# Performance work log

Hardware: AMD Instinct MI355X
Metric: run time of the kernel (lower is better)

## Reference

```python
import jax, jax.numpy as jnp
import numpy as np

CD_WEIGHT = 100.0


def setup_inputs() -> dict:
    key = jax.random.key(0)
    k1, k2 = jax.random.split(key)
    array1 = jax.random.normal(k1, (4, 4096, 3), dtype=jnp.float32)
    array2 = jax.random.normal(k2, (4, 4096, 3), dtype=jnp.float32)
    return {"array1": array1, "array2": array2}


def _chamfer(a1, a2):
    # a1: [B, N, D], a2: [B, M, D]
    # squared pairwise distances d2[b, n, m] = ||a1[b,n] - a2[b,m]||^2
    # computed as ||a||^2 + ||b||^2 - 2 a.b to avoid materializing [B,N,M,D]
    sq1 = jnp.sum(a1 * a1, axis=-1)                      # [B, N]
    sq2 = jnp.sum(a2 * a2, axis=-1)                      # [B, M]
    cross = jnp.einsum("bnd,bmd->bnm", a1, a2)           # [B, N, M]
    d2 = sq1[:, :, None] + sq2[:, None, :] - 2.0 * cross  # [B, N, M]
    # av_dist1: for each array2 point, min over array1 points, then mean
    av_dist1 = jnp.mean(jnp.min(d2, axis=1), axis=-1)    # [B]
    # av_dist2: for each array1 point, min over array2 points, then mean
    av_dist2 = jnp.mean(jnp.min(d2, axis=2), axis=-1)    # [B]
    return CD_WEIGHT * jnp.mean(0.5 * (av_dist1 + av_dist2))


def reference(array1, array2):
    return _chamfer(array1, array2)
```

## Files before the change

kernel.cpp:

```cpp
#include <hip/hip_runtime.h>
#include <math.h>


#define NPTS     4096
#define NBATCH   4
#define RSPLIT   32
#define RCHUNK   (NPTS / RSPLIT)
#define QPB      256
#define QPT      8
#define QBLK     (QPB * QPT)
#define NQTOT    (2 * NBATCH * NPTS)
#define SCALE    (50.0f / (float)(NBATCH * NPTS))

__global__ __launch_bounds__(QPB) void chamfer_stage1(
    const float* __restrict__ a1, const float* __restrict__ a2,
    float* __restrict__ pm)
{
    __shared__ float4 refs[RCHUNK];

    const int b   = blockIdx.y;
    const int dir = blockIdx.z >> 5;
    const int c   = blockIdx.z & 31;
    const float* q = (dir == 0) ? a1 : a2;
    const float* r = (dir == 0) ? a2 : a1;
    q += (size_t)b * NPTS * 3;
    r += (size_t)b * NPTS * 3;

    if (threadIdx.x < RCHUNK) {
        const int g = c * RCHUNK + threadIdx.x;
        float rx = r[3 * g + 0];
        float ry = r[3 * g + 1];
        float rz = r[3 * g + 2];
        refs[threadIdx.x] = make_float4(rx, ry, rz, rx * rx + ry * ry + rz * rz);
    }

    const int q0 = blockIdx.x * QBLK + threadIdx.x;
    float qx2[QPT], qy2[QPT], qz2[QPT], q2[QPT];
    #pragma unroll
    for (int k = 0; k < QPT; ++k) {
        const int qi = q0 + k * QPB;
        float x = q[3 * qi + 0];
        float y = q[3 * qi + 1];
        float z = q[3 * qi + 2];
        q2[k]  = x * x + y * y + z * z;
        qx2[k] = -2.0f * x;
        qy2[k] = -2.0f * y;
        qz2[k] = -2.0f * z;
    }
    __syncthreads();

    float mins[QPT];
    #pragma unroll
    for (int k = 0; k < QPT; ++k) mins[k] = INFINITY;

    #pragma unroll 2
    for (int j = 0; j < RCHUNK; ++j) {
        float4 p = refs[j];
        #pragma unroll
        for (int k = 0; k < QPT; ++k) {
            float t = fmaf(qz2[k], p.z,
                      fmaf(qy2[k], p.y,
                      fmaf(qx2[k], p.x, p.w)));
            mins[k] = fminf(mins[k], t);
        }
    }

    const int qgbase = (dir * NBATCH + b) * NPTS + q0;
    #pragma unroll
    for (int k = 0; k < QPT; ++k) {
        pm[(size_t)c * NQTOT + qgbase + k * QPB] = mins[k] + q2[k];
    }
}

__global__ __launch_bounds__(256) void chamfer_stage2(
    const float* __restrict__ pm, float* __restrict__ psum)
{
    const int qg = blockIdx.x * 256 + threadIdx.x;
    float m = INFINITY;
    #pragma unroll
    for (int c = 0; c < RSPLIT; ++c)
        m = fminf(m, pm[(size_t)c * NQTOT + qg]);

    float s = m;
    for (int off = 32; off > 0; off >>= 1) s += __shfl_down(s, off);
    __shared__ float wsum[4];
    if ((threadIdx.x & 63) == 0) wsum[threadIdx.x >> 6] = s;
    __syncthreads();
    if (threadIdx.x == 0)
        psum[blockIdx.x] = wsum[0] + wsum[1] + wsum[2] + wsum[3];
}

__global__ __launch_bounds__(64) void chamfer_stage3(
    const float* __restrict__ psum, float* __restrict__ out)
{
    float s = psum[threadIdx.x] + psum[threadIdx.x + 64];
    for (int off = 32; off > 0; off >>= 1) s += __shfl_down(s, off);
    if (threadIdx.x == 0) out[0] = s * SCALE;
}

extern "C" void kernel_launch(void* const* d_in, const int* in_sizes, int n_in,
                              void* d_out, int out_size, void* d_ws, size_t ws_size,
                              hipStream_t stream) {
    const float* a1 = (const float*)d_in[0];
    const float* a2 = (const float*)d_in[1];
    float* out  = (float*)d_out;
    float* pm   = (float*)d_ws;
    float* psum = (float*)((char*)d_ws + (size_t)RSPLIT * NQTOT * sizeof(float));

    chamfer_stage1<<<dim3(NPTS / QBLK, NBATCH, 2 * RSPLIT), QPB, 0, stream>>>(a1, a2, pm);
    chamfer_stage2<<<NQTOT / 256, 256, 0, stream>>>(pm, psum);
    chamfer_stage3<<<1, 64, 0, stream>>>(psum, out);
}
```

Measured before the change: 72.31 us.

## Fuse partial-min stage into main kernel with in-block reference split and shuffle reduction

Restructures the work split so each block owns 64 query points and loads the full 4096-point reference set into LDS. Four thread lanes cover 16 queries each, and 64 slices of the reference set are reduced with wave shuffles plus a small LDS merge. This removes the 32-way partial-min buffer in global memory and the separate stage-2 kernel, leaving two launches instead of three. In exchange, each block now loads all references with a padded LDS layout (about 66KB). Occupancy is limited to 2 blocks per CU, and the grid shrinks to 512 blocks.

```diff
diff --git a/kernel.cpp b/kernel.cpp
--- a/kernel.cpp
+++ b/kernel.cpp
@@ -4,58 +4,67 @@
 
 #define NPTS     4096
 #define NBATCH   4
-#define RSPLIT   32
-#define RCHUNK   (NPTS / RSPLIT)
 #define QPB      256
-#define QPT      8
-#define QBLK     (QPB * QPT)
-#define NQTOT    (2 * NBATCH * NPTS)
+#define QBLK     64
+#define QPT      16
+#define NSLICE   64
+#define RSLICE   (NPTS / NSLICE)
+#define SSTRIDE  65
+#define NBLK     (2 * NBATCH * (NPTS / QBLK))
 #define SCALE    (50.0f / (float)(NBATCH * NPTS))
 
-__global__ __launch_bounds__(QPB) void chamfer_stage1(
+__global__ __launch_bounds__(QPB, 2) void chamfer_main(
     const float* __restrict__ a1, const float* __restrict__ a2,
-    float* __restrict__ pm)
+    float* __restrict__ psum)
 {
-    __shared__ float4 refs[RCHUNK];
+    __shared__ float4 refs[NSLICE * SSTRIDE];
+    __shared__ float4 qlds[QBLK];
+    __shared__ float  pm2[4][QBLK];
 
-    const int b   = blockIdx.y;
-    const int dir = blockIdx.z >> 5;
-    const int c   = blockIdx.z & 31;
+    const int bid = blockIdx.x;
+    const int dir = bid >> 8;
+    const int b   = (bid >> 6) & 3;
+    const int qc  = bid & 63;
     const float* q = (dir == 0) ? a1 : a2;
     const float* r = (dir == 0) ? a2 : a1;
-    q += (size_t)b * NPTS * 3;
+    q += (size_t)b * NPTS * 3 + (size_t)qc * QBLK * 3;
     r += (size_t)b * NPTS * 3;
 
-    if (threadIdx.x < RCHUNK) {
-        const int g = c * RCHUNK + threadIdx.x;
+    const int tid = threadIdx.x;
+
+    for (int g = tid; g < NPTS; g += QPB) {
         float rx = r[3 * g + 0];
         float ry = r[3 * g + 1];
         float rz = r[3 * g + 2];
-        refs[threadIdx.x] = make_float4(rx, ry, rz, rx * rx + ry * ry + rz * rz);
+        refs[(g >> 6) * SSTRIDE + (g & 63)] =
+            make_float4(rx, ry, rz, rx * rx + ry * ry + rz * rz);
     }
+    if (tid < QBLK) {
+        float x = q[3 * tid + 0];
+        float y = q[3 * tid + 1];
+        float z = q[3 * tid + 2];
+        qlds[tid] = make_float4(-2.0f * x, -2.0f * y, -2.0f * z,
+                                x * x + y * y + z * z);
+    }
+    __syncthreads();
 
-    const int q0 = blockIdx.x * QBLK + threadIdx.x;
-    float qx2[QPT], qy2[QPT], qz2[QPT], q2[QPT];
+    const int qg = (tid & 3) * QPT;
+    const int s  = tid >> 2;
+    float qx2[QPT], qy2[QPT], qz2[QPT];
     #pragma unroll
     for (int k = 0; k < QPT; ++k) {
-        const int qi = q0 + k * QPB;
-        float x = q[3 * qi + 0];
-        float y = q[3 * qi + 1];
-        float z = q[3 * qi + 2];
-        q2[k]  = x * x + y * y + z * z;
-        qx2[k] = -2.0f * x;
-        qy2[k] = -2.0f * y;
-        qz2[k] = -2.0f * z;
+        float4 ql = qlds[qg + k];
+        qx2[k] = ql.x; qy2[k] = ql.y; qz2[k] = ql.z;
     }
-    __syncthreads();
 
     float mins[QPT];
     #pragma unroll
     for (int k = 0; k < QPT; ++k) mins[k] = INFINITY;
 
+    const float4* rp = &refs[s * SSTRIDE];
     #pragma unroll 2
-    for (int j = 0; j < RCHUNK; ++j) {
-        float4 p = refs[j];
+    for (int j = 0; j < RSLICE; ++j) {
+        float4 p = rp[j];
         #pragma unroll
         for (int k = 0; k < QPT; ++k) {
             float t = fmaf(qz2[k], p.z,
@@ -65,37 +74,39 @@
         }
     }
 
-    const int qgbase = (dir * NBATCH + b) * NPTS + q0;
     #pragma unroll
-    for (int k = 0; k < QPT; ++k) {
-        pm[(size_t)c * NQTOT + qgbase + k * QPB] = mins[k] + q2[k];
+    for (int m = 4; m <= 32; m <<= 1) {
+        #pragma unroll
+        for (int k = 0; k < QPT; ++k)
+            mins[k] = fminf(mins[k], __shfl_xor(mins[k], m));
+    }
+    const int wv = tid >> 6;
+    if ((tid & 63) < 4) {
+        #pragma unroll
+        for (int k = 0; k < QPT; ++k)
+            pm2[wv][qg + k] = mins[k];
+    }
+    __syncthreads();
+
+    if (tid < QBLK) {
+        float m = fminf(fminf(pm2[0][tid], pm2[1][tid]),
+                        fminf(pm2[2][tid], pm2[3][tid]));
+        float v = m + qlds[tid].w;
+        for (int off = 32; off > 0; off >>= 1) v += __shfl_down(v, off);
+        if (tid == 0) psum[bid] = v;
     }
 }
 
-__global__ __launch_bounds__(256) void chamfer_stage2(
-    const float* __restrict__ pm, float* __restrict__ psum)
+__global__ __launch_bounds__(256) void chamfer_final(
+    const float* __restrict__ psum, float* __restrict__ out)
 {
-    const int qg = blockIdx.x * 256 + threadIdx.x;
-    float m = INFINITY;
-    #pragma unroll
-    for (int c = 0; c < RSPLIT; ++c)
-        m = fminf(m, pm[(size_t)c * NQTOT + qg]);
-
-    float s = m;
+    float s = psum[threadIdx.x] + psum[threadIdx.x + 256];
     for (int off = 32; off > 0; off >>= 1) s += __shfl_down(s, off);
     __shared__ float wsum[4];
     if ((threadIdx.x & 63) == 0) wsum[threadIdx.x >> 6] = s;
     __syncthreads();
     if (threadIdx.x == 0)
-        psum[blockIdx.x] = wsum[0] + wsum[1] + wsum[2] + wsum[3];
-}
-
-__global__ __launch_bounds__(64) void chamfer_stage3(
-    const float* __restrict__ psum, float* __restrict__ out)
-{
-    float s = psum[threadIdx.x] + psum[threadIdx.x + 64];
-    for (int off = 32; off > 0; off >>= 1) s += __shfl_down(s, off);
-    if (threadIdx.x == 0) out[0] = s * SCALE;
+        out[0] = (wsum[0] + wsum[1] + wsum[2] + wsum[3]) * SCALE;
 }
 
 extern "C" void kernel_launch(void* const* d_in, const int* in_sizes, int n_in,
@@ -104,10 +115,8 @@
     const float* a1 = (const float*)d_in[0];
     const float* a2 = (const float*)d_in[1];
     float* out  = (float*)d_out;
-    float* pm   = (float*)d_ws;
-    float* psum = (float*)((char*)d_ws + (size_t)RSPLIT * NQTOT * sizeof(float));
+    float* psum = (float*)d_ws;
 
-    chamfer_stage1<<<dim3(NPTS / QBLK, NBATCH, 2 * RSPLIT), QPB, 0, stream>>>(a1, a2, pm);
-    chamfer_stage2<<<NQTOT / 256, 256, 0, stream>>>(pm, psum);
-    chamfer_stage3<<<1, 64, 0, stream>>>(psum, out);
+    chamfer_main<<<NBLK, QPB, 0, stream>>>(a1, a2, psum);
+    chamfer_final<<<1, 256, 0, stream>>>(psum, out);
 }
```

New measurement: 71.92 us. About the same (-0.5%).
